# Performance work log

Hardware: AMD Instinct MI355X
Metric: run time of the kernel (lower is better)

The kernel has to match this reference:

```python
import jax, jax.numpy as jnp
import numpy as np

GRID_SIZE = 5
SPLINE_ORDER = 3
COUPLING = 0.05
LN_EPS = 1e-5
BATCH = 1024
IN_DIM = 2048
HIDDEN = [4096, 4096, 2048]


def _knots():
    k = SPLINE_ORDER
    return np.concatenate([np.full(k, -1.0), np.linspace(-1.0, 1.0, GRID_SIZE + 1), np.full(k, 1.0)])


def bspline_basis(t):
    # Replicates the module's partial in-place Cox-de Boor recursion exactly:
    # after the loops, cols[0..4] are degree-3, col 5 degree-2, col 6 degree-1, col 7 degree-0.
    knots = _knots()
    k = SPLINE_ORDER
    n = len(knots) - k - 1  # 8
    cols = [jnp.where((t >= knots[i]) & (t < knots[i + 1]), 1.0, 0.0).astype(t.dtype)
            for i in range(min(n, len(knots) - 1))]
    for degree in range(1, min(k + 1, n)):
        for i in range(n - degree):
            denom1 = knots[i + degree] - knots[i]
            denom2 = knots[i + degree + 1] - knots[i + 1]
            term1 = ((t - knots[i]) / denom1) * cols[i] if denom1 > 1e-10 else 0.0
            term2 = (((knots[i + degree + 1] - t) / denom2) * cols[i + 1]
                     if (denom2 > 1e-10 and i + 1 < n) else 0.0)
            cols[i] = term1 + term2
    return jnp.stack(cols, axis=-1)  # [..., n]


def kan_activation(x, control_points, reg_weights):
    # x: [B, D]; control_points: [D, grid+order+1]; reg_weights: [D]
    t = jnp.tanh(x)
    basis = bspline_basis(t)  # [B, D, n]
    m = min(basis.shape[-1], control_points.shape[1])  # min(8, 9) = 8
    spline = jnp.einsum('bdn,dn->bd', basis[..., :m], control_points[:, :m])
    return jnp.clip(spline * reg_weights[None, :], -10.0, 10.0)


def _generators():
    sx = np.array([[0., 1.], [1., 0.]], np.float32)
    sy = np.array([[0., -1.], [1., 0.]], np.float32)
    sz = np.array([[1., 0.], [0., -1.]], np.float32)
    return np.stack([sx, sy, sz, np.eye(2, dtype=np.float32)])  # [4,2,2]

GENS = jnp.asarray(_generators())
GEN_DIAG = jnp.asarray(np.stack([np.diagonal(g) for g in _generators()]))  # [4,2]


def noncommutative_transform(x):
    # pairs of the flattened tensor, generator index cycles mod 4
    shape = x.shape
    flat = x.reshape(-1)
    P = flat.shape[0] // 2
    vec = flat[:2 * P].reshape(P, 2)
    ng = GENS.shape[0]
    if P % ng == 0:
        v = vec.reshape(P // ng, ng, 2)                      # [Q, 4, 2]
        gv = jnp.einsum('gij,qgj->qgi', GENS, v)
        vg = v * GEN_DIAG[None, :, :]
        comm = jnp.clip(gv - vg, -1.0, 1.0)
        out = (v + COUPLING * comm).reshape(-1)
    else:
        G = GENS[jnp.arange(P) % ng]
        gv = jnp.einsum('pij,pj->pi', G, vec)
        vg = vec * jnp.diagonal(G, axis1=-2, axis2=-1)
        comm = jnp.clip(gv - vg, -1.0, 1.0)
        out = (vec + COUPLING * comm).reshape(-1)
    if flat.shape[0] % 2 == 1:
        out = jnp.concatenate([out, flat[-1:]])
    return out.reshape(shape)


def setup_inputs() -> dict:
    key = jax.random.key(0)
    ks = jax.random.split(key, 16)
    inp = {'x': jax.random.normal(ks[0], (BATCH, IN_DIM), jnp.float32)}
    prev = IN_DIM
    ncp = GRID_SIZE + SPLINE_ORDER + 1  # 9
    for li, h in enumerate(HIDDEN, start=1):
        kw, kb, kc = jax.random.split(ks[li], 3)
        inp[f'W{li}'] = jax.random.normal(kw, (h, prev), jnp.float32) / np.sqrt(prev)
        inp[f'b{li}'] = jnp.zeros((h,), jnp.float32)
        inp[f'cp{li}'] = jax.random.normal(kc, (h, ncp), jnp.float32) * 0.1
        inp[f'rw{li}'] = jnp.full((h,), 0.5, jnp.float32)
        prev = h
    inp['W_out'] = jax.random.normal(ks[10], (IN_DIM, prev), jnp.float32) / np.sqrt(prev)
    inp['b_out'] = jnp.zeros((IN_DIM,), jnp.float32)
    return inp


def reference(x, W1, b1, cp1, rw1, W2, b2, cp2, rw2, W3, b3, cp3, rw3, W_out, b_out):
    # F.layer_norm over feature dim, no affine
    mu = jnp.mean(x, axis=-1, keepdims=True)
    var = jnp.var(x, axis=-1, keepdims=True)
    cur = (x - mu) / jnp.sqrt(var + LN_EPS)
    for W, b, cp, rw in ((W1, b1, cp1, rw1), (W2, b2, cp2, rw2), (W3, b3, cp3, rw3)):
        lin = cur @ W.T + b
        kan = kan_activation(lin, cp, rw)
        cur = noncommutative_transform(kan)  # dropout = identity in eval
    return cur @ W_out.T + b_out
```

## Files before the change

### kernel.cpp

```cpp
#include <hip/hip_runtime.h>

typedef __attribute__((ext_vector_type(8))) short bf16x8;
typedef __attribute__((ext_vector_type(4))) float f32x4;

__device__ __forceinline__ float b2f(unsigned short u) {
    union { unsigned int i; float f; } x; x.i = ((unsigned int)u) << 16; return x.f;
}
__device__ __forceinline__ unsigned short f2b(float f) {
    union { float f; unsigned int i; } x; x.f = f;
    unsigned int r = x.i + 0x7fffu + ((x.i >> 16) & 1u);
    return (unsigned short)(r >> 16);
}

__device__ __forceinline__ void gl16(unsigned short* l, const unsigned short* g) {
    __builtin_amdgcn_global_load_lds((__attribute__((address_space(1))) void*)g,
                                     (__attribute__((address_space(3))) void*)l, 16, 0, 0);
}

__device__ __forceinline__ float kan_spline(float t, const float* cpf, float rwf) {
    float c3 = (t >= -1.0f && t < -0.6f) ? 1.0f : 0.0f;
    float c4 = (t >= -0.6f && t < -0.2f) ? 1.0f : 0.0f;
    float c5 = (t >= -0.2f && t <  0.2f) ? 1.0f : 0.0f;
    float c6 = (t >=  0.2f && t <  0.6f) ? 1.0f : 0.0f;
    float c7 = (t >=  0.6f && t <  1.0f) ? 1.0f : 0.0f;
    float d2 = (-0.6f - t) * 2.5f * c3;
    float d3 = (t + 1.0f) * 2.5f * c3 + (-0.2f - t) * 2.5f * c4;
    float d4 = (t + 0.6f) * 2.5f * c4 + ( 0.2f - t) * 2.5f * c5;
    float d5 = (t + 0.2f) * 2.5f * c5 + ( 0.6f - t) * 2.5f * c6;
    float d6 = (t - 0.2f) * 2.5f * c6 + ( 1.0f - t) * 2.5f * c7;
    float e1 = (-0.6f - t) * 2.5f  * d2;
    float e2 = (t + 1.0f) * 2.5f  * d2 + (-0.2f - t) * 1.25f * d3;
    float e3 = (t + 1.0f) * 1.25f * d3 + ( 0.2f - t) * 1.25f * d4;
    float e4 = (t + 0.6f) * 1.25f * d4 + ( 0.6f - t) * 1.25f * d5;
    float e5 = (t + 0.2f) * 1.25f * d5 + ( 1.0f - t) * 1.25f * d6;
    const float r12 = 1.0f / 1.2f;
    float f0 = (-0.6f - t) * 2.5f  * e1;
    float f1 = (t + 1.0f) * 2.5f  * e1 + (-0.2f - t) * 1.25f * e2;
    float f2 = (t + 1.0f) * 1.25f * e2 + ( 0.2f - t) * r12   * e3;
    float f3 = (t + 1.0f) * r12   * e3 + ( 0.6f - t) * r12   * e4;
    float f4 = (t + 0.6f) * r12   * e4 + ( 1.0f - t) * r12   * e5;
    float sp = f0*cpf[0] + f1*cpf[1] + f2*cpf[2] + f3*cpf[3] + f4*cpf[4]
             + e5*cpf[5] + d6*cpf[6] + c7*cpf[7];
    float v = sp * rwf;
    return fminf(fmaxf(v, -10.0f), 10.0f);
}

__global__ void ln_stats_kernel(const float* __restrict__ x,
                                float* __restrict__ mu, float* __restrict__ rstd) {
    const int row = blockIdx.x;
    const float* p = x + (size_t)row * 2048 + threadIdx.x * 8;
    double s = 0.0, q = 0.0;
#pragma unroll
    for (int i = 0; i < 8; ++i) { float v = p[i]; s += v; q += (double)v * v; }
    for (int o = 32; o > 0; o >>= 1) { s += __shfl_down(s, o, 64); q += __shfl_down(q, o, 64); }
    __shared__ double shs[4], shq[4];
    const int lane = threadIdx.x & 63, w = threadIdx.x >> 6;
    if (lane == 0) { shs[w] = s; shq[w] = q; }
    __syncthreads();
    if (threadIdx.x == 0) {
        double S = shs[0] + shs[1] + shs[2] + shs[3];
        double Q = shq[0] + shq[1] + shq[2] + shq[3];
        double m = S / 2048.0;
        double var = Q / 2048.0 - m * m;
        mu[row] = (float)m;
        rstd[row] = (float)(1.0 / sqrt(var + 1e-5));
    }
}

__global__ void rowsum_kernel(const float* __restrict__ W,
                              float* __restrict__ S, int K) {
    const int lane = threadIdx.x & 63, w = threadIdx.x >> 6;
    const int row = blockIdx.x * 4 + w;
    const float* p = W + (size_t)row * K;
    double s = 0.0;
    for (int c = lane * 8; c < K; c += 512) {
#pragma unroll
        for (int i = 0; i < 8; ++i) s += p[c + i];
    }
    for (int o = 32; o > 0; o >>= 1) s += __shfl_down(s, o, 64);
    if (lane == 0) S[row] = (float)s;
}

__global__ void split2_kernel(const float* __restrict__ src,
                              unsigned short* __restrict__ dst, int C) {
    const int r = blockIdx.x;
    const int c = threadIdx.x * 8;
    const float* p = src + (size_t)r * C + c;
    float4 u0 = ((const float4*)p)[0];
    float4 u1 = ((const float4*)p)[1];
    float v[8] = {u0.x, u0.y, u0.z, u0.w, u1.x, u1.y, u1.z, u1.w};
    unsigned short hi[8], lo[8];
#pragma unroll
    for (int i = 0; i < 8; ++i) {
        hi[i] = f2b(v[i]);
        lo[i] = f2b(v[i] - b2f(hi[i]));
    }
    unsigned short* d = dst + (size_t)r * 2 * C + c;
    *(uint4*)d = *(const uint4*)hi;
    *(uint4*)(d + C) = *(const uint4*)lo;
}

__global__ void pre_all(const float* __restrict__ x, const float* __restrict__ W1,
                        float* __restrict__ mu, float* __restrict__ rstd,
                        float* __restrict__ S1,
                        unsigned short* __restrict__ Asplit,
                        unsigned short* __restrict__ W1b) {
    const int tid = threadIdx.x;
    const int lane = tid & 63, w = tid >> 6;
    const int c = tid * 8;
    __shared__ double shs[4], shq[4];
    if (blockIdx.x < 1024) {
        const int r = blockIdx.x;
        const float* p = x + (size_t)r * 2048 + c;
        float4 u0 = ((const float4*)p)[0];
        float4 u1 = ((const float4*)p)[1];
        float v[8] = {u0.x, u0.y, u0.z, u0.w, u1.x, u1.y, u1.z, u1.w};
        double s = 0.0, q = 0.0;
#pragma unroll
        for (int i = 0; i < 8; ++i) { s += v[i]; q += (double)v[i] * v[i]; }
        for (int o = 32; o > 0; o >>= 1) { s += __shfl_down(s, o, 64); q += __shfl_down(q, o, 64); }
        if (lane == 0) { shs[w] = s; shq[w] = q; }
        __syncthreads();
        if (tid == 0) {
            double S = shs[0] + shs[1] + shs[2] + shs[3];
            double Q = shq[0] + shq[1] + shq[2] + shq[3];
            double m = S / 2048.0;
            double var = Q / 2048.0 - m * m;
            mu[r] = (float)m;
            rstd[r] = (float)(1.0 / sqrt(var + 1e-5));
        }
        unsigned short hi[8], lo[8];
#pragma unroll
        for (int i = 0; i < 8; ++i) {
            hi[i] = f2b(v[i]);
            lo[i] = f2b(v[i] - b2f(hi[i]));
        }
        unsigned short* d = Asplit + (size_t)r * 4096 + c;
        *(uint4*)d = *(const uint4*)hi;
        *(uint4*)(d + 2048) = *(const uint4*)lo;
    } else {
        const int r = blockIdx.x - 1024;
        const float* p = W1 + (size_t)r * 2048 + c;
        float4 u0 = ((const float4*)p)[0];
        float4 u1 = ((const float4*)p)[1];
        float v[8] = {u0.x, u0.y, u0.z, u0.w, u1.x, u1.y, u1.z, u1.w};
        double s = 0.0;
#pragma unroll
        for (int i = 0; i < 8; ++i) s += v[i];
        for (int o = 32; o > 0; o >>= 1) s += __shfl_down(s, o, 64);
        if (lane == 0) shs[w] = s;
        __syncthreads();
        if (tid == 0) S1[r] = (float)(shs[0] + shs[1] + shs[2] + shs[3]);
        unsigned short hi[8], lo[8];
#pragma unroll
        for (int i = 0; i < 8; ++i) {
            hi[i] = f2b(v[i]);
            lo[i] = f2b(v[i] - b2f(hi[i]));
        }
        unsigned short* d = W1b + (size_t)r * 4096 + c;
        *(uint4*)d = *(const uint4*)hi;
        *(uint4*)(d + 2048) = *(const uint4*)lo;
    }
}

__global__ void cvt_kernel(const float* __restrict__ src,
                           unsigned short* __restrict__ dst) {
    const size_t i = ((size_t)blockIdx.x * 256 + threadIdx.x) * 8;
    float4 u0 = ((const float4*)(src + i))[0];
    float4 u1 = ((const float4*)(src + i))[1];
    float v[8] = {u0.x, u0.y, u0.z, u0.w, u1.x, u1.y, u1.z, u1.w};
    unsigned short t[8];
#pragma unroll
    for (int q = 0; q < 8; ++q) t[q] = f2b(v[q]);
    *(uint4*)(dst + i) = *(const uint4*)t;
}

__global__ void cvt2_kernel(const float* __restrict__ s1, unsigned short* __restrict__ d1,
                            int nb1, const float* __restrict__ s2,
                            unsigned short* __restrict__ d2) {
    const int b = blockIdx.x;
    const float* src = (b < nb1) ? s1 : s2;
    unsigned short* dst = (b < nb1) ? d1 : d2;
    const int bb = (b < nb1) ? b : b - nb1;
    const size_t i = ((size_t)bb * 256 + threadIdx.x) * 8;
    float4 u0 = ((const float4*)(src + i))[0];
    float4 u1 = ((const float4*)(src + i))[1];
    float v[8] = {u0.x, u0.y, u0.z, u0.w, u1.x, u1.y, u1.z, u1.w};
    unsigned short t[8];
#pragma unroll
    for (int q = 0; q < 8; ++q) t[q] = f2b(v[q]);
    *(uint4*)(dst + i) = *(const uint4*)t;
}

template <int EPI>
__global__ __launch_bounds__(256, 2)
void gemm_kan2(const unsigned short* __restrict__ Ab,
               const unsigned short* __restrict__ Bb,
               const float* __restrict__ bias, const float* __restrict__ cp,
               const float* __restrict__ rw, const float* __restrict__ mu,
               const float* __restrict__ rstd, const float* __restrict__ S1,
               void* __restrict__ outp,
               int Nld, int n0, int Ktot, int lda, int ldb)
{
    constexpr int BM = 64, BN = 128, BK = 64;
    constexpr int ASZ = BM * BK;
    constexpr int BUF = ASZ + BN * BK;
    __shared__ unsigned short lds[3 * BUF];

    const int tid  = threadIdx.x;
    const int lane = tid & 63;
    const int wid  = tid >> 6;

    const int gx = gridDim.x;
    int flat = blockIdx.y * gx + blockIdx.x;
    const int nwg = gx * gridDim.y;
    if ((nwg & 7) == 0) flat = (flat & 7) * (nwg >> 3) + (flat >> 3);
    const int bm = (flat % gx) * BM;
    const int bn = (flat / gx) * BN;

    const int wmo = (wid >> 1) * 32;
    const int wno = (wid & 1) * 64;
    const int fr = lane & 15;
    const int kq = lane >> 4;
    const int sxr = fr & 7;

    const int uA0 = (wid << 7) + lane;
    const int uA1 = uA0 + 64;
    const int uB0 = (wid << 8) + lane;
    const int uB1 = uB0 + 64, uB2 = uB0 + 128, uB3 = uB0 + 192;
#define SRCOL(u) (((((u) & 7) ^ (((u) >> 3) & 7))) << 3)
    const size_t aoff0 = (size_t)(bm + (uA0 >> 3)) * lda + SRCOL(uA0);
    const size_t aoff1 = (size_t)(bm + (uA1 >> 3)) * lda + SRCOL(uA1);
    const size_t boff0 = (size_t)(bn + (uB0 >> 3)) * ldb + SRCOL(uB0);
    const size_t boff1 = (size_t)(bn + (uB1 >> 3)) * ldb + SRCOL(uB1);
    const size_t boff2 = (size_t)(bn + (uB2 >> 3)) * ldb + SRCOL(uB2);
    const size_t boff3 = (size_t)(bn + (uB3 >> 3)) * ldb + SRCOL(uB3);
#undef SRCOL

    f32x4 acc[2][4] = {};

#define STAGE(BSEL, AK, BKK) do {                                     \
    unsigned short* lA_ = &lds[(BSEL) * BUF];                         \
    unsigned short* lB_ = lA_ + ASZ;                                  \
    gl16(lA_ + uA0 * 8, Ab + aoff0 + (AK));                           \
    gl16(lA_ + uA1 * 8, Ab + aoff1 + (AK));                           \
    gl16(lB_ + uB0 * 8, Bb + boff0 + (BKK));                          \
    gl16(lB_ + uB1 * 8, Bb + boff1 + (BKK));                          \
    gl16(lB_ + uB2 * 8, Bb + boff2 + (BKK));                          \
    gl16(lB_ + uB3 * 8, Bb + boff3 + (BKK));                          \
} while (0)

    const int nt = Ktot / BK;
    STAGE(0, 0, 0);
    STAGE(1, BK, BK);

    for (int t = 0; t < nt; ++t) {
        if (t + 1 < nt) asm volatile("s_waitcnt vmcnt(6)" ::: "memory");
        else            asm volatile("s_waitcnt vmcnt(0)" ::: "memory");
        __builtin_amdgcn_s_barrier();
        __builtin_amdgcn_sched_barrier(0);
        if (t + 2 < nt) {
            const int kn = (t + 2) * BK;
            int ak = kn, bk = kn;
            if (EPI == 0) {
                ak = (kn < 4096) ? kn : kn - 4096;
                bk = (kn < 2048) ? kn : kn - 2048;
            }
            STAGE((t + 2) % 3, ak, bk);
        }
        const unsigned short* cl = &lds[(t % 3) * BUF];
#pragma unroll
        for (int s = 0; s < 2; ++s) {
            const int sl = ((((s << 2) + kq) ^ sxr)) << 3;
            bf16x8 aF[2], bF[4];
#pragma unroll
            for (int i = 0; i < 2; ++i)
                aF[i] = *(const bf16x8*)&cl[(wmo + i * 16 + fr) * BK + sl];
#pragma unroll
            for (int j = 0; j < 4; ++j)
                bF[j] = *(const bf16x8*)&cl[ASZ + (wno + j * 16 + fr) * BK + sl];
#pragma unroll
            for (int i = 0; i < 2; ++i)
#pragma unroll
                for (int j = 0; j < 4; ++j)
                    acc[i][j] = __builtin_amdgcn_mfma_f32_16x16x32_bf16(aF[i], bF[j], acc[i][j], 0, 0, 0);
        }
    }
#undef STAGE

    const int rowg = (lane >> 4) * 4;
#pragma unroll
    for (int j = 0; j < 4; ++j) {
        const int n = n0 + bn + wno + j * 16 + fr;
        const float bs = bias[n];
        float cpf[8], rwf = 0.0f, s1 = 0.0f;
        if (EPI < 2) {
#pragma unroll
            for (int q = 0; q < 8; ++q) cpf[q] = cp[(size_t)n * 9 + q];
            rwf = rw[n];
        }
        if (EPI == 0) s1 = S1[n];
        const int s = n & 7;
#pragma unroll
        for (int i = 0; i < 2; ++i) {
            const int m0 = bm + wmo + i * 16 + rowg;
#pragma unroll
            for (int r = 0; r < 4; ++r) {
                const int m = m0 + r;
                float v = acc[i][j][r];
                if (EPI == 0) v = (v - mu[m] * s1) * rstd[m] + bs;
                else          v += bs;
                if (EPI < 2) {
                    v = kan_spline(tanhf(v), cpf, rwf);
                    float p = __shfl_xor(v, 1, 64);
                    p = fminf(fmaxf(p, -1.0f), 1.0f);
                    if (s < 4) v += ((s == 2) ? -0.05f : 0.05f) * p;
                }
                if (EPI == 2) ((float*)outp)[(size_t)m * Nld + n] = v;
                else ((unsigned short*)outp)[(size_t)m * Nld + n] = f2b(v);
            }
        }
    }
}

template <int EPI, int BSRC>
__global__ __launch_bounds__(256, 2)
void gemm_kan(const void* __restrict__ Av, const void* __restrict__ Bv,
              const float* __restrict__ bias, const float* __restrict__ cp,
              const float* __restrict__ rw, const float* __restrict__ mu,
              const float* __restrict__ rstd, const float* __restrict__ S1,
              void* __restrict__ outp,
              int Nld, int n0, int Ktot, int lda, int ldb)
{
    constexpr int BM = 64, BN = 64, BK = 64, LDP = 72;
    constexpr bool SPL = (BSRC == 2);
    constexpr int OFF_B  = BM * LDP;
    constexpr int OFF_LO = (BM + BN) * LDP;
    __shared__ unsigned short lds[(SPL ? 2 : 1) * (BM + BN) * LDP];

    const int tid  = threadIdx.x;
    const int lane = tid & 63;
    const int wid  = tid >> 6;
    const int bm = blockIdx.x * BM;
    const int bn = blockIdx.y * BN;
    const int wmo = (wid >> 1) * 32;
    const int wno = (wid & 1) * 32;
    const int fr = lane & 15;
    const int kq = lane >> 4;
    const int sar = tid >> 3, sac = (tid & 7) << 3;
    const int sfr = tid >> 2, sfc = (tid & 3) << 4;

    f32x4 acc[2][2] = {};

    uint4 pA0 = {}, pA1 = {}, pB0 = {}, pB1 = {};
    const unsigned short* Ab = (const unsigned short*)Av;
    const unsigned short* Bb = (const unsigned short*)Bv;
    const size_t a0 = (size_t)(bm + sar) * lda + sac;
    const size_t a1 = (size_t)(bm + 32 + sar) * lda + sac;
    const size_t b0 = (size_t)(bn + sar) * ldb + sac;
    const size_t b1 = (size_t)(bn + 32 + sar) * ldb + sac;
    if constexpr (BSRC == 0) {
        pA0 = *(const uint4*)(Ab + a0);
        pA1 = *(const uint4*)(Ab + a1);
        pB0 = *(const uint4*)(Bb + b0);
        pB1 = *(const uint4*)(Bb + b1);
    }

    for (int k0 = 0; k0 < Ktot; k0 += BK) {
        if constexpr (BSRC == 0) {
            *(uint4*)&lds[sar * LDP + sac] = pA0;
            *(uint4*)&lds[(32 + sar) * LDP + sac] = pA1;
            *(uint4*)&lds[OFF_B + sar * LDP + sac] = pB0;
            *(uint4*)&lds[OFF_B + (32 + sar) * LDP + sac] = pB1;
        } else {
            {
                const float* g = (const float*)Bv + (size_t)(bn + sfr) * ldb + k0 + sfc;
                float4 u0 = ((const float4*)g)[0];
                float4 u1 = ((const float4*)g)[1];
                float4 u2 = ((const float4*)g)[2];
                float4 u3 = ((const float4*)g)[3];
                float v[16] = {u0.x,u0.y,u0.z,u0.w, u1.x,u1.y,u1.z,u1.w,
                               u2.x,u2.y,u2.z,u2.w, u3.x,u3.y,u3.z,u3.w};
                unsigned short hi[16], lo[16];
#pragma unroll
                for (int i = 0; i < 16; ++i) {
                    hi[i] = f2b(v[i]);
                    if (SPL) lo[i] = f2b(v[i] - b2f(hi[i]));
                }
                unsigned short* d = &lds[OFF_B + sfr * LDP + sfc];
                ((uint4*)d)[0] = *(const uint4*)&hi[0];
                ((uint4*)d)[1] = *(const uint4*)&hi[8];
                if constexpr (SPL) {
                    unsigned short* dl = d + OFF_LO;
                    ((uint4*)dl)[0] = *(const uint4*)&lo[0];
                    ((uint4*)dl)[1] = *(const uint4*)&lo[8];
                }
            }
            if constexpr (SPL) {
                const float* g = (const float*)Av + (size_t)(bm + sfr) * lda + k0 + sfc;
                float4 u0 = ((const float4*)g)[0];
                float4 u1 = ((const float4*)g)[1];
                float4 u2 = ((const float4*)g)[2];
                float4 u3 = ((const float4*)g)[3];
                float v[16] = {u0.x,u0.y,u0.z,u0.w, u1.x,u1.y,u1.z,u1.w,
                               u2.x,u2.y,u2.z,u2.w, u3.x,u3.y,u3.z,u3.w};
                unsigned short hi[16], lo[16];
#pragma unroll
                for (int i = 0; i < 16; ++i) {
                    hi[i] = f2b(v[i]);
                    lo[i] = f2b(v[i] - b2f(hi[i]));
                }
                unsigned short* d = &lds[sfr * LDP + sfc];
                ((uint4*)d)[0] = *(const uint4*)&hi[0];
                ((uint4*)d)[1] = *(const uint4*)&hi[8];
                unsigned short* dl = d + OFF_LO;
                ((uint4*)dl)[0] = *(const uint4*)&lo[0];
                ((uint4*)dl)[1] = *(const uint4*)&lo[8];
            } else {
                *(uint4*)&lds[sar * LDP + sac] = *(const uint4*)(Ab + a0 + k0);
                *(uint4*)&lds[(32 + sar) * LDP + sac] = *(const uint4*)(Ab + a1 + k0);
            }
        }
        __syncthreads();
        if constexpr (BSRC == 0) {
            if (k0 + BK < Ktot) {
                const int kn = k0 + BK;
                const int ak = (EPI == 0) ? (kn < 4096 ? kn : kn - 4096) : kn;
                const int bk = (EPI == 0) ? (kn < 2048 ? kn : kn - 2048) : kn;
                pA0 = *(const uint4*)(Ab + a0 + ak);
                pA1 = *(const uint4*)(Ab + a1 + ak);
                pB0 = *(const uint4*)(Bb + b0 + bk);
                pB1 = *(const uint4*)(Bb + b1 + bk);
            }
        }
#pragma unroll
        for (int s = 0; s < 2; ++s) {
            const int cc = (s * 4 + kq) << 3;
            bf16x8 aF[2], bF[2];
#pragma unroll
            for (int i = 0; i < 2; ++i)
                aF[i] = *(const bf16x8*)&lds[(wmo + i * 16 + fr) * LDP + cc];
#pragma unroll
            for (int j = 0; j < 2; ++j)
                bF[j] = *(const bf16x8*)&lds[OFF_B + (wno + j * 16 + fr) * LDP + cc];
#pragma unroll
            for (int i = 0; i < 2; ++i)
#pragma unroll
                for (int j = 0; j < 2; ++j)
                    acc[i][j] = __builtin_amdgcn_mfma_f32_16x16x32_bf16(aF[i], bF[j], acc[i][j], 0, 0, 0);
            if constexpr (SPL) {
                bf16x8 aL[2], bL[2];
#pragma unroll
                for (int i = 0; i < 2; ++i)
                    aL[i] = *(const bf16x8*)&lds[OFF_LO + (wmo + i * 16 + fr) * LDP + cc];
#pragma unroll
                for (int i = 0; i < 2; ++i)
#pragma unroll
                    for (int j = 0; j < 2; ++j)
                        acc[i][j] = __builtin_amdgcn_mfma_f32_16x16x32_bf16(aL[i], bF[j], acc[i][j], 0, 0, 0);
#pragma unroll
                for (int j = 0; j < 2; ++j)
                    bL[j] = *(const bf16x8*)&lds[OFF_LO + OFF_B + (wno + j * 16 + fr) * LDP + cc];
#pragma unroll
                for (int i = 0; i < 2; ++i)
#pragma unroll
                    for (int j = 0; j < 2; ++j)
                        acc[i][j] = __builtin_amdgcn_mfma_f32_16x16x32_bf16(aF[i], bL[j], acc[i][j], 0, 0, 0);
            }
        }
        __syncthreads();
    }

    const int rowg = (lane >> 4) * 4;
#pragma unroll
    for (int j = 0; j < 2; ++j) {
        const int n = n0 + bn + wno + j * 16 + fr;
        const float bs = bias[n];
        float cpf[8], rwf = 0.0f, s1 = 0.0f;
        if (EPI < 2) {
#pragma unroll
            for (int q = 0; q < 8; ++q) cpf[q] = cp[(size_t)n * 9 + q];
            rwf = rw[n];
        }
        if (EPI == 0) s1 = S1[n];
        const int s = n & 7;
#pragma unroll
        for (int i = 0; i < 2; ++i) {
            const int m0 = bm + wmo + i * 16 + rowg;
#pragma unroll
            for (int r = 0; r < 4; ++r) {
                const int m = m0 + r;
                float v = acc[i][j][r];
                if (EPI == 0) v = (v - mu[m] * s1) * rstd[m] + bs;
                else          v += bs;
                if (EPI < 2) {
                    v = kan_spline(tanhf(v), cpf, rwf);
                    float p = __shfl_xor(v, 1, 64);
                    p = fminf(fmaxf(p, -1.0f), 1.0f);
                    if (s < 4) v += ((s == 2) ? -0.05f : 0.05f) * p;
                }
                if (EPI == 2) ((float*)outp)[(size_t)m * Nld + n] = v;
                else ((unsigned short*)outp)[(size_t)m * Nld + n] = f2b(v);
            }
        }
    }
}

extern "C" void kernel_launch(void* const* d_in, const int* in_sizes, int n_in,
                              void* d_out, int out_size, void* d_ws, size_t ws_size,
                              hipStream_t stream) {
    const float* x    = (const float*)d_in[0];
    const float* W1   = (const float*)d_in[1];
    const float* b1   = (const float*)d_in[2];
    const float* cp1  = (const float*)d_in[3];
    const float* rw1  = (const float*)d_in[4];
    const float* W2   = (const float*)d_in[5];
    const float* b2   = (const float*)d_in[6];
    const float* cp2  = (const float*)d_in[7];
    const float* rw2  = (const float*)d_in[8];
    const float* W3   = (const float*)d_in[9];
    const float* b3   = (const float*)d_in[10];
    const float* cp3  = (const float*)d_in[11];
    const float* rw3  = (const float*)d_in[12];
    const float* Wout = (const float*)d_in[13];
    const float* bout = (const float*)d_in[14];

    char* ws = (char*)d_ws;
    float* mu   = (float*)(ws);
    float* rstd = (float*)(ws + 4096);
    float* S1   = (float*)(ws + 8192);
    unsigned short* A2 = (unsigned short*)(ws + 32768);
    unsigned short* A3 = (unsigned short*)(ws + 32768 + 8388608);
    unsigned short* A4 = A2;
    unsigned short* Asplit = A3;
    unsigned short* Wb = (unsigned short*)(ws + 32768 + 2 * 8388608);
    const size_t NEED_FULL = 32768 + 2 * 8388608 + 33554432;
    const size_t NEED_HALF = 32768 + 2 * 8388608 + 16777216;

    if (ws_size >= NEED_FULL) {
        pre_all<<<5120, 256, 0, stream>>>(x, W1, mu, rstd, S1, Asplit, Wb);
        gemm_kan2<0><<<dim3(16, 32), 256, 0, stream>>>(
            Asplit, Wb, b1, cp1, rw1, mu, rstd, S1, A2, 4096, 0, 6144, 4096, 4096);
        cvt_kernel<<<8192, 256, 0, stream>>>(W2, Wb);
        gemm_kan2<1><<<dim3(16, 32), 256, 0, stream>>>(
            A2, Wb, b2, cp2, rw2, nullptr, nullptr, nullptr, A3, 4096, 0, 4096, 4096, 4096);
        cvt2_kernel<<<6144, 256, 0, stream>>>(W3, Wb, 4096, Wout, Wb + 8388608);
        gemm_kan2<1><<<dim3(16, 16), 256, 0, stream>>>(
            A3, Wb, b3, cp3, rw3, nullptr, nullptr, nullptr, A4, 2048, 0, 4096, 4096, 4096);
        gemm_kan2<2><<<dim3(16, 16), 256, 0, stream>>>(
            A4, Wb + 8388608, bout, nullptr, nullptr, nullptr, nullptr, nullptr, d_out, 2048, 0, 2048, 2048, 2048);
    } else if (ws_size >= NEED_HALF) {
        ln_stats_kernel<<<1024, 256, 0, stream>>>(x, mu, rstd);
        rowsum_kernel<<<1024, 256, 0, stream>>>(W1, S1, 2048);
        split2_kernel<<<1024, 256, 0, stream>>>(x, Asplit, 2048);
        for (int h = 0; h < 2; ++h) {
            split2_kernel<<<2048, 256, 0, stream>>>(W1 + (size_t)h * 2048 * 2048, Wb, 2048);
            gemm_kan2<0><<<dim3(16, 16), 256, 0, stream>>>(
                Asplit, Wb, b1, cp1, rw1, mu, rstd, S1, A2, 4096, h * 2048, 6144, 4096, 4096);
        }
        for (int h = 0; h < 2; ++h) {
            cvt_kernel<<<4096, 256, 0, stream>>>(W2 + (size_t)h * 2048 * 4096, Wb);
            gemm_kan2<1><<<dim3(16, 16), 256, 0, stream>>>(
                A2, Wb, b2, cp2, rw2, nullptr, nullptr, nullptr, A3, 4096, h * 2048, 4096, 4096, 4096);
        }
        cvt_kernel<<<4096, 256, 0, stream>>>(W3, Wb);
        gemm_kan2<1><<<dim3(16, 16), 256, 0, stream>>>(
            A3, Wb, b3, cp3, rw3, nullptr, nullptr, nullptr, A4, 2048, 0, 4096, 4096, 4096);
        cvt_kernel<<<2048, 256, 0, stream>>>(Wout, Wb);
        gemm_kan2<2><<<dim3(16, 16), 256, 0, stream>>>(
            A4, Wb, bout, nullptr, nullptr, nullptr, nullptr, nullptr, d_out, 2048, 0, 2048, 2048, 2048);
    } else {
        ln_stats_kernel<<<1024, 256, 0, stream>>>(x, mu, rstd);
        rowsum_kernel<<<1024, 256, 0, stream>>>(W1, S1, 2048);
        gemm_kan<0, 2><<<dim3(16, 64), 256, 0, stream>>>(
            x, W1, b1, cp1, rw1, mu, rstd, S1, A2, 4096, 0, 2048, 2048, 2048);
        gemm_kan<1, 1><<<dim3(16, 64), 256, 0, stream>>>(
            A2, W2, b2, cp2, rw2, nullptr, nullptr, nullptr, A3, 4096, 0, 4096, 4096, 4096);
        gemm_kan<1, 1><<<dim3(16, 32), 256, 0, stream>>>(
            A3, W3, b3, cp3, rw3, nullptr, nullptr, nullptr, A4, 2048, 0, 4096, 4096, 4096);
        gemm_kan<2, 1><<<dim3(16, 32), 256, 0, stream>>>(
            A4, Wout, bout, nullptr, nullptr, nullptr, nullptr, nullptr, d_out, 2048, 0, 2048, 2048, 2048);
    }
}
```

Before: 382.7 us.

## Split-K the last two GEMMs with separate reduce-and-epilogue kernels

```diff
diff --git a/kernel.cpp b/kernel.cpp
--- a/kernel.cpp
+++ b/kernel.cpp
@@ -192,6 +192,48 @@
     *(uint4*)(dst + i) = *(const uint4*)t;
 }
 
+template <int RK>
+__global__ void reduce_epi(const float* __restrict__ P0, const float* __restrict__ P1,
+                           const float* __restrict__ bias,
+                           const float* __restrict__ cp, const float* __restrict__ rw,
+                           void* __restrict__ outp, int N) {
+    const int m = blockIdx.x;
+    const int c0 = threadIdx.x * 8;
+    const float* p0 = P0 + (size_t)m * N + c0;
+    const float* p1 = P1 + (size_t)m * N + c0;
+    float4 a0 = ((const float4*)p0)[0], a1 = ((const float4*)p0)[1];
+    float4 b0 = ((const float4*)p1)[0], b1 = ((const float4*)p1)[1];
+    float v[8] = {a0.x + b0.x, a0.y + b0.y, a0.z + b0.z, a0.w + b0.w,
+                  a1.x + b1.x, a1.y + b1.y, a1.z + b1.z, a1.w + b1.w};
+#pragma unroll
+    for (int i = 0; i < 8; ++i) v[i] += bias[c0 + i];
+    if constexpr (RK == 1) {
+        float w[8];
+#pragma unroll
+        for (int i = 0; i < 8; ++i) {
+            const int n = c0 + i;
+            float cpf[8];
+#pragma unroll
+            for (int q = 0; q < 8; ++q) cpf[q] = cp[(size_t)n * 9 + q];
+            w[i] = kan_spline(tanhf(v[i]), cpf, rw[n]);
+        }
+        unsigned short o[8];
+#pragma unroll
+        for (int i = 0; i < 8; ++i) {
+            float val = w[i];
+            const int s = i;
+            float p = fminf(fmaxf(w[i ^ 1], -1.0f), 1.0f);
+            if (s < 4) val += ((s == 2) ? -0.05f : 0.05f) * p;
+            o[i] = f2b(val);
+        }
+        *(uint4*)((unsigned short*)outp + (size_t)m * N + c0) = *(const uint4*)o;
+    } else {
+        float* o = (float*)outp + (size_t)m * N + c0;
+        ((float4*)o)[0] = make_float4(v[0], v[1], v[2], v[3]);
+        ((float4*)o)[1] = make_float4(v[4], v[5], v[6], v[7]);
+    }
+}
+
 template <int EPI>
 __global__ __launch_bounds__(256, 2)
 void gemm_kan2(const unsigned short* __restrict__ Ab,
@@ -200,7 +242,7 @@
                const float* __restrict__ rw, const float* __restrict__ mu,
                const float* __restrict__ rstd, const float* __restrict__ S1,
                void* __restrict__ outp,
-               int Nld, int n0, int Ktot, int lda, int ldb)
+               int Nld, int n0, int Ktot, int lda, int ldb, int nbn, int khoff)
 {
     constexpr int BM = 64, BN = 128, BK = 64;
     constexpr int ASZ = BM * BK;
@@ -216,7 +258,10 @@
     const int nwg = gx * gridDim.y;
     if ((nwg & 7) == 0) flat = (flat & 7) * (nwg >> 3) + (flat >> 3);
     const int bm = (flat % gx) * BM;
-    const int bn = (flat / gx) * BN;
+    const int rest = flat / gx;
+    const int bn = (rest % nbn) * BN;
+    const int kh = rest / nbn;
+    const int koff = kh * Ktot;
 
     const int wmo = (wid >> 1) * 32;
     const int wno = (wid & 1) * 64;
@@ -229,12 +274,12 @@
     const int uB0 = (wid << 8) + lane;
     const int uB1 = uB0 + 64, uB2 = uB0 + 128, uB3 = uB0 + 192;
 #define SRCOL(u) (((((u) & 7) ^ (((u) >> 3) & 7))) << 3)
-    const size_t aoff0 = (size_t)(bm + (uA0 >> 3)) * lda + SRCOL(uA0);
-    const size_t aoff1 = (size_t)(bm + (uA1 >> 3)) * lda + SRCOL(uA1);
-    const size_t boff0 = (size_t)(bn + (uB0 >> 3)) * ldb + SRCOL(uB0);
-    const size_t boff1 = (size_t)(bn + (uB1 >> 3)) * ldb + SRCOL(uB1);
-    const size_t boff2 = (size_t)(bn + (uB2 >> 3)) * ldb + SRCOL(uB2);
-    const size_t boff3 = (size_t)(bn + (uB3 >> 3)) * ldb + SRCOL(uB3);
+    const size_t aoff0 = (size_t)(bm + (uA0 >> 3)) * lda + SRCOL(uA0) + koff;
+    const size_t aoff1 = (size_t)(bm + (uA1 >> 3)) * lda + SRCOL(uA1) + koff;
+    const size_t boff0 = (size_t)(bn + (uB0 >> 3)) * ldb + SRCOL(uB0) + koff;
+    const size_t boff1 = (size_t)(bn + (uB1 >> 3)) * ldb + SRCOL(uB1) + koff;
+    const size_t boff2 = (size_t)(bn + (uB2 >> 3)) * ldb + SRCOL(uB2) + koff;
+    const size_t boff3 = (size_t)(bn + (uB3 >> 3)) * ldb + SRCOL(uB3) + koff;
 #undef SRCOL
 
     f32x4 acc[2][4] = {};
@@ -292,14 +337,14 @@
 #pragma unroll
     for (int j = 0; j < 4; ++j) {
         const int n = n0 + bn + wno + j * 16 + fr;
-        const float bs = bias[n];
-        float cpf[8], rwf = 0.0f, s1 = 0.0f;
-        if (EPI < 2) {
+        float bs = 0.0f, cpf[8], rwf = 0.0f, s1 = 0.0f;
+        if constexpr (EPI < 3) bs = bias[n];
+        if constexpr (EPI < 2) {
 #pragma unroll
             for (int q = 0; q < 8; ++q) cpf[q] = cp[(size_t)n * 9 + q];
             rwf = rw[n];
         }
-        if (EPI == 0) s1 = S1[n];
+        if constexpr (EPI == 0) s1 = S1[n];
         const int s = n & 7;
 #pragma unroll
         for (int i = 0; i < 2; ++i) {
@@ -308,15 +353,16 @@
             for (int r = 0; r < 4; ++r) {
                 const int m = m0 + r;
                 float v = acc[i][j][r];
-                if (EPI == 0) v = (v - mu[m] * s1) * rstd[m] + bs;
-                else          v += bs;
-                if (EPI < 2) {
+                if constexpr (EPI == 0) v = (v - mu[m] * s1) * rstd[m] + bs;
+                else if constexpr (EPI < 3) v += bs;
+                if constexpr (EPI < 2) {
                     v = kan_spline(tanhf(v), cpf, rwf);
                     float p = __shfl_xor(v, 1, 64);
                     p = fminf(fmaxf(p, -1.0f), 1.0f);
                     if (s < 4) v += ((s == 2) ? -0.05f : 0.05f) * p;
                 }
-                if (EPI == 2) ((float*)outp)[(size_t)m * Nld + n] = v;
+                if constexpr (EPI == 2)      ((float*)outp)[(size_t)m * Nld + n] = v;
+                else if constexpr (EPI == 3) ((float*)outp)[(size_t)kh * khoff + (size_t)m * Nld + n] = v;
                 else ((unsigned short*)outp)[(size_t)m * Nld + n] = f2b(v);
             }
         }
@@ -531,45 +577,55 @@
     float* S1   = (float*)(ws + 8192);
     unsigned short* A2 = (unsigned short*)(ws + 32768);
     unsigned short* A3 = (unsigned short*)(ws + 32768 + 8388608);
-    unsigned short* A4 = A2;
     unsigned short* Asplit = A3;
     unsigned short* Wb = (unsigned short*)(ws + 32768 + 2 * 8388608);
+    float* Pk0 = (float*)(ws + 32768);
+    const int KHOFF = 10582016;
+    unsigned short* A4v = A3;
     const size_t NEED_FULL = 32768 + 2 * 8388608 + 33554432;
     const size_t NEED_HALF = 32768 + 2 * 8388608 + 16777216;
 
     if (ws_size >= NEED_FULL) {
         pre_all<<<5120, 256, 0, stream>>>(x, W1, mu, rstd, S1, Asplit, Wb);
         gemm_kan2<0><<<dim3(16, 32), 256, 0, stream>>>(
-            Asplit, Wb, b1, cp1, rw1, mu, rstd, S1, A2, 4096, 0, 6144, 4096, 4096);
+            Asplit, Wb, b1, cp1, rw1, mu, rstd, S1, A2, 4096, 0, 6144, 4096, 4096, 32, 0);
         cvt_kernel<<<8192, 256, 0, stream>>>(W2, Wb);
         gemm_kan2<1><<<dim3(16, 32), 256, 0, stream>>>(
-            A2, Wb, b2, cp2, rw2, nullptr, nullptr, nullptr, A3, 4096, 0, 4096, 4096, 4096);
+            A2, Wb, b2, cp2, rw2, nullptr, nullptr, nullptr, A3, 4096, 0, 4096, 4096, 4096, 32, 0);
         cvt2_kernel<<<6144, 256, 0, stream>>>(W3, Wb, 4096, Wout, Wb + 8388608);
-        gemm_kan2<1><<<dim3(16, 16), 256, 0, stream>>>(
-            A3, Wb, b3, cp3, rw3, nullptr, nullptr, nullptr, A4, 2048, 0, 4096, 4096, 4096);
-        gemm_kan2<2><<<dim3(16, 16), 256, 0, stream>>>(
-            A4, Wb + 8388608, bout, nullptr, nullptr, nullptr, nullptr, nullptr, d_out, 2048, 0, 2048, 2048, 2048);
+        gemm_kan2<3><<<dim3(16, 32), 256, 0, stream>>>(
+            A3, Wb, nullptr, nullptr, nullptr, nullptr, nullptr, nullptr,
+            Pk0, 2048, 0, 2048, 4096, 4096, 16, KHOFF);
+        reduce_epi<1><<<1024, 256, 0, stream>>>(
+            Pk0, Pk0 + KHOFF, b3, cp3, rw3, A4v, 2048);
+        gemm_kan2<3><<<dim3(16, 32), 256, 0, stream>>>(
+            A4v, Wb + 8388608, nullptr, nullptr, nullptr, nullptr, nullptr, nullptr,
+            Pk0, 2048, 0, 1024, 2048, 2048, 16, KHOFF);
+        reduce_epi<2><<<1024, 256, 0, stream>>>(
+            Pk0, Pk0 + KHOFF, bout, nullptr, nullptr, d_out, 2048);
     } else if (ws_size >= NEED_HALF) {
+        unsigned short* A4 = A2;
         ln_stats_kernel<<<1024, 256, 0, stream>>>(x, mu, rstd);
         rowsum_kernel<<<1024, 256, 0, stream>>>(W1, S1, 2048);
         split2_kernel<<<1024, 256, 0, stream>>>(x, Asplit, 2048);
         for (int h = 0; h < 2; ++h) {
             split2_kernel<<<2048, 256, 0, stream>>>(W1 + (size_t)h * 2048 * 2048, Wb, 2048);
             gemm_kan2<0><<<dim3(16, 16), 256, 0, stream>>>(
-                Asplit, Wb, b1, cp1, rw1, mu, rstd, S1, A2, 4096, h * 2048, 6144, 4096, 4096);
+                Asplit, Wb, b1, cp1, rw1, mu, rstd, S1, A2, 4096, h * 2048, 6144, 4096, 4096, 16, 0);
         }
         for (int h = 0; h < 2; ++h) {
             cvt_kernel<<<4096, 256, 0, stream>>>(W2 + (size_t)h * 2048 * 4096, Wb);
             gemm_kan2<1><<<dim3(16, 16), 256, 0, stream>>>(
-                A2, Wb, b2, cp2, rw2, nullptr, nullptr, nullptr, A3, 4096, h * 2048, 4096, 4096, 4096);
+                A2, Wb, b2, cp2, rw2, nullptr, nullptr, nullptr, A3, 4096, h * 2048, 4096, 4096, 4096, 16, 0);
         }
         cvt_kernel<<<4096, 256, 0, stream>>>(W3, Wb);
         gemm_kan2<1><<<dim3(16, 16), 256, 0, stream>>>(
-            A3, Wb, b3, cp3, rw3, nullptr, nullptr, nullptr, A4, 2048, 0, 4096, 4096, 4096);
+            A3, Wb, b3, cp3, rw3, nullptr, nullptr, nullptr, A4, 2048, 0, 4096, 4096, 4096, 16, 0);
         cvt_kernel<<<2048, 256, 0, stream>>>(Wout, Wb);
         gemm_kan2<2><<<dim3(16, 16), 256, 0, stream>>>(
-            A4, Wb, bout, nullptr, nullptr, nullptr, nullptr, nullptr, d_out, 2048, 0, 2048, 2048, 2048);
+            A4, Wb, bout, nullptr, nullptr, nullptr, nullptr, nullptr, d_out, 2048, 0, 2048, 2048, 2048, 16, 0);
     } else {
+        unsigned short* A4 = A2;
         ln_stats_kernel<<<1024, 256, 0, stream>>>(x, mu, rstd);
         rowsum_kernel<<<1024, 256, 0, stream>>>(W1, S1, 2048);
         gemm_kan<0, 2><<<dim3(16, 64), 256, 0, stream>>>(
```

After: 393.1 us. +2.7%, slower.

## Add dedicated split-bf16 layer-1 GEMM reusing hi/lo tiles across three MFMA passes

Applied to the files above, without the earlier changes.

```diff
diff --git a/kernel.cpp b/kernel.cpp
--- a/kernel.cpp
+++ b/kernel.cpp
@@ -192,6 +192,126 @@
     *(uint4*)(dst + i) = *(const uint4*)t;
 }
 
+__global__ __launch_bounds__(256, 2)
+void gemm_kan1(const unsigned short* __restrict__ Ab,
+               const unsigned short* __restrict__ Bb,
+               const float* __restrict__ bias, const float* __restrict__ cp,
+               const float* __restrict__ rw, const float* __restrict__ mu,
+               const float* __restrict__ rstd, const float* __restrict__ S1,
+               unsigned short* __restrict__ outp,
+               int Nld, int Klog, int lda, int ldb)
+{
+    constexpr int BM = 64, BN = 128, BK = 32;
+    constexpr int AHI = 0, ALO = 2048, BHI = 4096, BLO = 8192;
+    constexpr int BUF = 12288;
+    __shared__ unsigned short lds[3 * BUF];
+
+    const int tid  = threadIdx.x;
+    const int lane = tid & 63;
+    const int wid  = tid >> 6;
+
+    const int gx = gridDim.x;
+    int flat = blockIdx.y * gx + blockIdx.x;
+    const int nwg = gx * gridDim.y;
+    if ((nwg & 7) == 0) flat = (flat & 7) * (nwg >> 3) + (flat >> 3);
+    const int bm = (flat % gx) * BM;
+    const int bn = (flat / gx) * BN;
+
+    const int wmo = (wid >> 1) * 32;
+    const int wno = (wid & 1) * 64;
+    const int fr = lane & 15;
+    const int kq = lane >> 4;
+    const int slotr = (kq ^ (fr & 3)) << 3;
+
+    const int rA = tid >> 2, sA = tid & 3;
+    const int rB1 = rA + 64;
+    const size_t aoff  = (size_t)(bm + rA)  * lda + ((sA ^ (rA  & 3)) << 3);
+    const size_t boff0 = (size_t)(bn + rA)  * ldb + ((sA ^ (rA  & 3)) << 3);
+    const size_t boff1 = (size_t)(bn + rB1) * ldb + ((sA ^ (rB1 & 3)) << 3);
+
+    f32x4 acc[2][4] = {};
+
+#define STAGE(BSEL, K) do {                                           \
+    unsigned short* l_ = &lds[(BSEL) * BUF];                          \
+    gl16(l_ + AHI + tid * 8,         Ab + aoff  + (K));               \
+    gl16(l_ + ALO + tid * 8,         Ab + aoff  + 2048 + (K));        \
+    gl16(l_ + BHI + tid * 8,         Bb + boff0 + (K));               \
+    gl16(l_ + BHI + (tid + 256) * 8, Bb + boff1 + (K));               \
+    gl16(l_ + BLO + tid * 8,         Bb + boff0 + 2048 + (K));        \
+    gl16(l_ + BLO + (tid + 256) * 8, Bb + boff1 + 2048 + (K));        \
+} while (0)
+
+    const int nt = Klog / BK;
+    STAGE(0, 0);
+    STAGE(1, BK);
+
+    for (int t = 0; t < nt; ++t) {
+        if (t + 1 < nt) asm volatile("s_waitcnt vmcnt(6)" ::: "memory");
+        else            asm volatile("s_waitcnt vmcnt(0)" ::: "memory");
+        __builtin_amdgcn_s_barrier();
+        __builtin_amdgcn_sched_barrier(0);
+        if (t + 2 < nt) STAGE((t + 2) % 3, (t + 2) * BK);
+        const unsigned short* cl = &lds[(t % 3) * BUF];
+        bf16x8 aH[2], aL[2], bH[4], bL[4];
+#pragma unroll
+        for (int i = 0; i < 2; ++i) {
+            const int ro = (wmo + i * 16 + fr) * 32 + slotr;
+            aH[i] = *(const bf16x8*)&cl[AHI + ro];
+            aL[i] = *(const bf16x8*)&cl[ALO + ro];
+        }
+#pragma unroll
+        for (int j = 0; j < 4; ++j) {
+            const int ro = (wno + j * 16 + fr) * 32 + slotr;
+            bH[j] = *(const bf16x8*)&cl[BHI + ro];
+            bL[j] = *(const bf16x8*)&cl[BLO + ro];
+        }
+#pragma unroll
+        for (int i = 0; i < 2; ++i)
+#pragma unroll
+            for (int j = 0; j < 4; ++j)
+                acc[i][j] = __builtin_amdgcn_mfma_f32_16x16x32_bf16(aH[i], bH[j], acc[i][j], 0, 0, 0);
+#pragma unroll
+        for (int i = 0; i < 2; ++i)
+#pragma unroll
+            for (int j = 0; j < 4; ++j)
+                acc[i][j] = __builtin_amdgcn_mfma_f32_16x16x32_bf16(aL[i], bH[j], acc[i][j], 0, 0, 0);
+#pragma unroll
+        for (int i = 0; i < 2; ++i)
+#pragma unroll
+            for (int j = 0; j < 4; ++j)
+                acc[i][j] = __builtin_amdgcn_mfma_f32_16x16x32_bf16(aH[i], bL[j], acc[i][j], 0, 0, 0);
+    }
+#undef STAGE
+
+    const int rowg = (lane >> 4) * 4;
+#pragma unroll
+    for (int j = 0; j < 4; ++j) {
+        const int n = bn + wno + j * 16 + fr;
+        const float bs = bias[n];
+        float cpf[8];
+#pragma unroll
+        for (int q = 0; q < 8; ++q) cpf[q] = cp[(size_t)n * 9 + q];
+        const float rwf = rw[n];
+        const float s1 = S1[n];
+        const int s = n & 7;
+#pragma unroll
+        for (int i = 0; i < 2; ++i) {
+            const int m0 = bm + wmo + i * 16 + rowg;
+#pragma unroll
+            for (int r = 0; r < 4; ++r) {
+                const int m = m0 + r;
+                float v = acc[i][j][r];
+                v = (v - mu[m] * s1) * rstd[m] + bs;
+                v = kan_spline(tanhf(v), cpf, rwf);
+                float p = __shfl_xor(v, 1, 64);
+                p = fminf(fmaxf(p, -1.0f), 1.0f);
+                if (s < 4) v += ((s == 2) ? -0.05f : 0.05f) * p;
+                outp[(size_t)m * Nld + n] = f2b(v);
+            }
+        }
+    }
+}
+
 template <int EPI>
 __global__ __launch_bounds__(256, 2)
 void gemm_kan2(const unsigned short* __restrict__ Ab,
@@ -539,8 +659,8 @@
 
     if (ws_size >= NEED_FULL) {
         pre_all<<<5120, 256, 0, stream>>>(x, W1, mu, rstd, S1, Asplit, Wb);
-        gemm_kan2<0><<<dim3(16, 32), 256, 0, stream>>>(
-            Asplit, Wb, b1, cp1, rw1, mu, rstd, S1, A2, 4096, 0, 6144, 4096, 4096);
+        gemm_kan1<<<dim3(16, 32), 256, 0, stream>>>(
+            Asplit, Wb, b1, cp1, rw1, mu, rstd, S1, A2, 4096, 2048, 4096, 4096);
         cvt_kernel<<<8192, 256, 0, stream>>>(W2, Wb);
         gemm_kan2<1><<<dim3(16, 32), 256, 0, stream>>>(
             A2, Wb, b2, cp2, rw2, nullptr, nullptr, nullptr, A3, 4096, 0, 4096, 4096, 4096);
```

After: 381.1 us. No clear change (-0.4%).
